# Performance work log

Hardware: AMD Instinct MI355X
Metric: run time of the kernel (lower is better)

Reference implementation:

```python
import jax, jax.numpy as jnp
import numpy as np

N_NODES = 100000
N_EDGES = 500000
HIDDEN = 32
HEADS = 4
PROJ = HIDDEN * HEADS  # 128
LN_EPS = 1e-5


def setup_inputs() -> dict:
    key = jax.random.key(0)
    ks = jax.random.split(key, 12)
    # Xavier-uniform bound for Linear(3, PROJ): sqrt(6/(3+PROJ))
    b_qkv = float(np.sqrt(6.0 / (3 + PROJ)))
    b_out = float(np.sqrt(6.0 / (PROJ + HIDDEN)))
    return {
        "positions": jax.random.normal(ks[0], (N_NODES, 3), dtype=jnp.float32),
        "edge_index": jax.random.randint(ks[1], (2, N_EDGES), 0, N_NODES, dtype=jnp.int64),
        "Wq": jax.random.uniform(ks[2], (3, PROJ), jnp.float32, -b_qkv, b_qkv),
        "bq": jnp.zeros((PROJ,), jnp.float32),
        "Wk": jax.random.uniform(ks[3], (3, PROJ), jnp.float32, -b_qkv, b_qkv),
        "bk": jnp.zeros((PROJ,), jnp.float32),
        "Wv": jax.random.uniform(ks[4], (3, PROJ), jnp.float32, -b_qkv, b_qkv),
        "bv": jnp.zeros((PROJ,), jnp.float32),
        "Wout": jax.random.uniform(ks[5], (PROJ, HIDDEN), jnp.float32, -b_out, b_out),
        "bout": jnp.zeros((HIDDEN,), jnp.float32),
        "gamma": jnp.ones((HIDDEN,), jnp.float32),
        "beta": jnp.zeros((HIDDEN,), jnp.float32),
    }


def reference(positions, edge_index, Wq, bq, Wk, bk, Wv, bv, Wout, bout, gamma, beta):
    row, col = edge_index[0], edge_index[1]
    rel = positions[row] - positions[col]                      # [E, 3]
    E = rel.shape[0]
    q = (rel @ Wq + bq).reshape(E, HEADS, HIDDEN)              # [E, H, D]
    k = (rel @ Wk + bk).reshape(E, HEADS, HIDDEN)
    v = (rel @ Wv + bv).reshape(E, HEADS, HIDDEN)
    # attention score per (edge, head), softmax over heads
    scores = jnp.sum(q * k, axis=-1) / jnp.sqrt(jnp.float32(HIDDEN))  # [E, H]
    attn = jax.nn.softmax(scores, axis=-1)                     # dropout is identity in eval
    wv = (attn[..., None] * v).reshape(E, PROJ)                # [E, H*D]
    # scatter-mean over destination nodes (col), dim_size = N
    seg_sum = jax.ops.segment_sum(wv, col, num_segments=N_NODES)
    counts = jax.ops.segment_sum(jnp.ones((E,), wv.dtype), col, num_segments=N_NODES)
    mean = seg_sum / jnp.maximum(counts, 1.0)[:, None]         # [N, H*D]
    out = mean @ Wout + bout                                   # [N, D]
    mu = jnp.mean(out, axis=-1, keepdims=True)
    var = jnp.var(out, axis=-1, keepdims=True)
    out = (out - mu) / jnp.sqrt(var + LN_EPS) * gamma + beta
    return jax.nn.silu(out)
```

## Files before the change

kernel.cpp:

```cpp
#include <hip/hip_runtime.h>
#include <hip/hip_fp16.h>

#define LN_EPS 1e-5f

typedef _Float16 f16x2 __attribute__((ext_vector_type(2)));
typedef _Float16 f16x8 __attribute__((ext_vector_type(8)));

__device__ __forceinline__ void pk_atomic_add_u32(_Float16* p, unsigned bits) {
  f16x2 v = __builtin_bit_cast(f16x2, bits);
#if __has_builtin(__builtin_amdgcn_flat_atomic_fadd_v2f16)
  __builtin_amdgcn_flat_atomic_fadd_v2f16((f16x2*)p, v);
#else
  unsafeAtomicAdd((__half2*)p, *(__half2*)&v);
#endif
}

__device__ __forceinline__ unsigned pack2(float a, float b) {
  f16x2 v;
  v.x = (_Float16)a;
  v.y = (_Float16)b;
  return __builtin_bit_cast(unsigned, v);
}


__global__ __launch_bounds__(128) void precompute_kernel(
    const float* __restrict__ Wq, const float* __restrict__ bq,
    const float* __restrict__ Wk, const float* __restrict__ bk,
    const float* __restrict__ Wv, const float* __restrict__ bv,
    const float* __restrict__ Wout, float* __restrict__ coef,
    float* __restrict__ T) {
  __shared__ float sW[1024];
  __shared__ float sM[4][3][32];
  __shared__ float sCv[4][32];
  const int t = threadIdx.x;
  const float scale = 0.17677669529663687f;

  if (blockIdx.x == 0) {
    for (int i = t; i < 384; i += 128) {
      sW[i] = Wq[i];
      sW[384 + i] = Wk[i];
    }
    sW[768 + t] = bq[t];
    sW[896 + t] = bk[t];
    __syncthreads();

    if (t < 40) {
      const int h = t / 10, j = t % 10;
      float acc = 0.f;
#pragma unroll 4
      for (int d = 0; d < 32; ++d) {
        const int idx = h * 32 + d;
        float q0 = sW[idx], q1 = sW[128 + idx], q2 = sW[256 + idx];
        float k0 = sW[384 + idx], k1 = sW[512 + idx], k2 = sW[640 + idx];
        float bqv = sW[768 + idx], bkv = sW[896 + idx];
        float v;
        switch (j) {
          case 0: v = q0 * k0; break;
          case 1: v = q1 * k1; break;
          case 2: v = q2 * k2; break;
          case 3: v = q0 * k1 + q1 * k0; break;
          case 4: v = q0 * k2 + q2 * k0; break;
          case 5: v = q1 * k2 + q2 * k1; break;
          case 6: v = q0 * bkv + k0 * bqv; break;
          case 7: v = q1 * bkv + k1 * bqv; break;
          case 8: v = q2 * bkv + k2 * bqv; break;
          default: v = bqv * bkv; break;
        }
        acc += v;
      }
      coef[t] = acc * scale;
    }
  } else {
    const int h = t >> 5, o = t & 31;
    float m0 = 0, m1 = 0, m2 = 0, cv = 0;
    for (int d = 0; d < 32; ++d) {
      const int j = h * 32 + d;
      const float w = Wout[j * 32 + o];
      m0 += Wv[j] * w;
      m1 += Wv[128 + j] * w;
      m2 += Wv[256 + j] * w;
      cv += bv[j] * w;
    }
    sM[h][0][o] = m0;
    sM[h][1][o] = m1;
    sM[h][2][o] = m2;
    sCv[h][o] = cv;
    __syncthreads();

    for (int idx = t; idx < 512; idx += 128) {
      const int j = idx >> 5, col = idx & 31;
      float v;
      if (j < 3)        v = sCv[j][col] - sCv[3][col];
      else if (j < 6)   v = sM[3][j - 3][col];
      else if (j < 15)  { const int h2 = (j - 6) / 3, i = (j - 6) % 3; v = sM[h2][i][col] - sM[3][i][col]; }
      else              v = sCv[3][col];
      T[idx] = v;
    }
  }
}

__global__ __launch_bounds__(256) void edge_kernel(
    const float* __restrict__ pos, const int* __restrict__ ei, int E,
    const float* __restrict__ coef, _Float16* __restrict__ fsums) {
  __shared__ unsigned sF[8][264];
  __shared__ int sC[256];

  const int t = threadIdx.x;
  const int lane64 = t & 63;

  bool pz = true;
  if (lane64 < 8) pz = (ei[2 * lane64 + 1] == 0);
  const unsigned long long bz = __ballot(pz);
  const int i64 = (int)__builtin_amdgcn_readfirstlane(bz == ~0ull ? 1 : 0);

  const int base = blockIdx.x * 256;
  const int vb = min(256, E - base);
  const int e = base + t;

  int c = 0;
  float px0 = 0, px1 = 0, px2 = 0, pc0 = 0, pc1 = 0, pc2 = 0;
  if (t < vb) {
    int r;
    if (i64) {
      r = ((const int2*)ei)[(size_t)e].x;
      c = ((const int2*)ei)[(size_t)E + (size_t)e].x;
    } else {
      r = ei[e];
      c = ei[(size_t)E + e];
    }
    px0 = pos[r * 3 + 0]; px1 = pos[r * 3 + 1]; px2 = pos[r * 3 + 2];
    pc0 = pos[c * 3 + 0]; pc1 = pos[c * 3 + 1]; pc2 = pos[c * 3 + 2];
  }

  if (t < vb) {
    const float rx = px0 - pc0;
    const float ry = px1 - pc1;
    const float rz = px2 - pc2;
    float s[4];
#pragma unroll
    for (int h = 0; h < 4; ++h) {
      const float* cf = coef + h * 10;
      s[h] = cf[9] + rx * cf[6] + ry * cf[7] + rz * cf[8] + rx * rx * cf[0] +
             ry * ry * cf[1] + rz * rz * cf[2] + rx * ry * cf[3] +
             rx * rz * cf[4] + ry * rz * cf[5];
    }
    const float mx = fmaxf(fmaxf(s[0], s[1]), fmaxf(s[2], s[3]));
    const float e0 = __expf(s[0] - mx), e1 = __expf(s[1] - mx);
    const float e2 = __expf(s[2] - mx), e3 = __expf(s[3] - mx);
    const float inv = 1.0f / (e0 + e1 + e2 + e3);
    const float a0 = e0 * inv, a1 = e1 * inv, a2 = e2 * inv;

    sC[t] = c;
    sF[0][t] = pack2(a0, a1);
    sF[1][t] = pack2(a2, rx);
    sF[2][t] = pack2(ry, rz);
    sF[3][t] = pack2(a0 * rx, a0 * ry);
    sF[4][t] = pack2(a0 * rz, a1 * rx);
    sF[5][t] = pack2(a1 * ry, a1 * rz);
    sF[6][t] = pack2(a2 * rx, a2 * ry);
    sF[7][t] = pack2(a2 * rz, 1.0f);
  }
  __syncthreads();

  const int w = t >> 6;
  const int slot = lane64 & 7;
  const int esub = lane64 >> 3;
#pragma unroll
  for (int i = 0; i < 8; ++i) {
    const int g = w * 64 + i * 8 + esub;
    if (g < vb) {
      const int ct = sC[g];
      const unsigned val = sF[slot][g];
      pk_atomic_add_u32(fsums + (size_t)ct * 16 + 2 * slot, val);
    }
  }
}

__global__ __launch_bounds__(256) void node_kernel(
    const _Float16* __restrict__ fsums, const float* __restrict__ T,
    const float* __restrict__ bout, const float* __restrict__ gamma,
    const float* __restrict__ beta, float* __restrict__ out, int N) {
  const int tid = blockIdx.x * blockDim.x + threadIdx.x;
  const int node = tid >> 5;
  const int col = tid & 31;
  if (node >= N) return;

  const f16x8* fp = (const f16x8*)(fsums + (size_t)node * 16);
  const f16x8 va = fp[0];
  const f16x8 vb = fp[1];
  float f[16];
#pragma unroll
  for (int j = 0; j < 8; ++j) {
    f[j] = (float)va[j];
    f[8 + j] = (float)vb[j];
  }
  const float invc = 1.0f / fmaxf(f[15], 1.0f);

  float acc = 0.f;
#pragma unroll
  for (int j = 0; j < 16; ++j) acc = fmaf(f[j], T[j * 32 + col], acc);
  acc = fmaf(acc, invc, bout[col]);

  float sx = acc, sx2 = acc * acc;
#pragma unroll
  for (int off = 16; off >= 1; off >>= 1) {
    sx += __shfl_xor(sx, off);
    sx2 += __shfl_xor(sx2, off);
  }
  const float mu = sx * (1.0f / 32.0f);
  const float var = sx2 * (1.0f / 32.0f) - mu * mu;
  const float inv = rsqrtf(var + LN_EPS);
  const float y = (acc - mu) * inv * gamma[col] + beta[col];
  const float o = y * (1.0f / (1.0f + __expf(-y)));
  out[(size_t)node * 32 + col] = o;
}

extern "C" void kernel_launch(void* const* d_in, const int* in_sizes, int n_in,
                              void* d_out, int out_size, void* d_ws, size_t ws_size,
                              hipStream_t stream) {
  const float* pos  = (const float*)d_in[0];
  const int*   ei   = (const int*)d_in[1];
  const float* Wq   = (const float*)d_in[2];
  const float* bq   = (const float*)d_in[3];
  const float* Wk   = (const float*)d_in[4];
  const float* bk   = (const float*)d_in[5];
  const float* Wv   = (const float*)d_in[6];
  const float* bv   = (const float*)d_in[7];
  const float* Wout = (const float*)d_in[8];
  const float* bout = (const float*)d_in[9];
  const float* gam  = (const float*)d_in[10];
  const float* bet  = (const float*)d_in[11];

  const int N = in_sizes[0] / 3;
  const int E = in_sizes[1] / 2;

  _Float16* fsums = (_Float16*)d_ws;
  float* coef = (float*)((char*)d_ws + (size_t)N * 32);
  float* T = coef + 48;

  hipMemsetAsync(fsums, 0, (size_t)N * 32, stream);

  precompute_kernel<<<2, 128, 0, stream>>>(Wq, bq, Wk, bk, Wv, bv, Wout, coef, T);

  const int edge_blocks = (E + 255) / 256;
  edge_kernel<<<edge_blocks, 256, 0, stream>>>(pos, ei, E, coef, fsums);

  const int node_blocks = (int)(((size_t)N * 32 + 255) / 256);
  node_kernel<<<node_blocks, 256, 0, stream>>>(fsums, T, bout, gam, bet,
                                               (float*)d_out, N);

  (void)n_in; (void)out_size; (void)ws_size;
}
```

Before: 136.7 us.

## Replicate fp16 accumulators across edge blocks and fuse zeroing into precompute kernel

Edge blocks now scatter their atomic adds into one of four replicated fp16 accumulator buffers, chosen by block index, which is meant to reduce atomic contention on the same node addresses. The node kernel sums the four replicas before the projection. The separate memset is replaced by zeroing done inside the precompute kernel, which now launches extra blocks for it. The cost is four times the accumulator memory to zero and read, with more memory traffic and a larger working set.

```diff
diff --git a/kernel.cpp b/kernel.cpp
--- a/kernel.cpp
+++ b/kernel.cpp
@@ -2,6 +2,7 @@
 #include <hip/hip_fp16.h>
 
 #define LN_EPS 1e-5f
+#define NREP 4
 
 typedef _Float16 f16x2 __attribute__((ext_vector_type(2)));
 typedef _Float16 f16x8 __attribute__((ext_vector_type(8)));
@@ -23,12 +24,12 @@
 }
 
 
-__global__ __launch_bounds__(128) void precompute_kernel(
+__global__ __launch_bounds__(256) void precompute_kernel(
     const float* __restrict__ Wq, const float* __restrict__ bq,
     const float* __restrict__ Wk, const float* __restrict__ bk,
     const float* __restrict__ Wv, const float* __restrict__ bv,
     const float* __restrict__ Wout, float* __restrict__ coef,
-    float* __restrict__ T) {
+    float* __restrict__ T, uint4* __restrict__ zbase, int zcount) {
   __shared__ float sW[1024];
   __shared__ float sM[4][3][32];
   __shared__ float sCv[4][32];
@@ -36,12 +37,14 @@
   const float scale = 0.17677669529663687f;
 
   if (blockIdx.x == 0) {
-    for (int i = t; i < 384; i += 128) {
+    for (int i = t; i < 384; i += 256) {
       sW[i] = Wq[i];
       sW[384 + i] = Wk[i];
     }
-    sW[768 + t] = bq[t];
-    sW[896 + t] = bk[t];
+    if (t < 128) {
+      sW[768 + t] = bq[t];
+      sW[896 + t] = bk[t];
+    }
     __syncthreads();
 
     if (t < 40) {
@@ -70,38 +73,47 @@
       }
       coef[t] = acc * scale;
     }
+  } else if (blockIdx.x == 1) {
+    if (t < 128) {
+      const int h = t >> 5, o = t & 31;
+      float m0 = 0, m1 = 0, m2 = 0, cv = 0;
+      for (int d = 0; d < 32; ++d) {
+        const int j = h * 32 + d;
+        const float w = Wout[j * 32 + o];
+        m0 += Wv[j] * w;
+        m1 += Wv[128 + j] * w;
+        m2 += Wv[256 + j] * w;
+        cv += bv[j] * w;
+      }
+      sM[h][0][o] = m0;
+      sM[h][1][o] = m1;
+      sM[h][2][o] = m2;
+      sCv[h][o] = cv;
+    }
+    __syncthreads();
+
+    if (t < 128) {
+      for (int idx = t; idx < 512; idx += 128) {
+        const int j = idx >> 5, col = idx & 31;
+        float v;
+        if (j < 3)        v = sCv[j][col] - sCv[3][col];
+        else if (j < 6)   v = sM[3][j - 3][col];
+        else if (j < 15)  { const int h2 = (j - 6) / 3, i = (j - 6) % 3; v = sM[h2][i][col] - sM[3][i][col]; }
+        else              v = sCv[3][col];
+        T[idx] = v;
+      }
+    }
   } else {
-    const int h = t >> 5, o = t & 31;
-    float m0 = 0, m1 = 0, m2 = 0, cv = 0;
-    for (int d = 0; d < 32; ++d) {
-      const int j = h * 32 + d;
-      const float w = Wout[j * 32 + o];
-      m0 += Wv[j] * w;
-      m1 += Wv[128 + j] * w;
-      m2 += Wv[256 + j] * w;
-      cv += bv[j] * w;
-    }
-    sM[h][0][o] = m0;
-    sM[h][1][o] = m1;
-    sM[h][2][o] = m2;
-    sCv[h][o] = cv;
-    __syncthreads();
-
-    for (int idx = t; idx < 512; idx += 128) {
-      const int j = idx >> 5, col = idx & 31;
-      float v;
-      if (j < 3)        v = sCv[j][col] - sCv[3][col];
-      else if (j < 6)   v = sM[3][j - 3][col];
-      else if (j < 15)  { const int h2 = (j - 6) / 3, i = (j - 6) % 3; v = sM[h2][i][col] - sM[3][i][col]; }
-      else              v = sCv[3][col];
-      T[idx] = v;
-    }
+    const uint4 z = {0u, 0u, 0u, 0u};
+    const int stride = (gridDim.x - 2) * 256;
+    for (int i = (blockIdx.x - 2) * 256 + t; i < zcount; i += stride)
+      zbase[i] = z;
   }
 }
 
 __global__ __launch_bounds__(256) void edge_kernel(
     const float* __restrict__ pos, const int* __restrict__ ei, int E,
-    const float* __restrict__ coef, _Float16* __restrict__ fsums) {
+    const float* __restrict__ coef, _Float16* __restrict__ fsums, int N) {
   __shared__ unsigned sF[8][264];
   __shared__ int sC[256];
 
@@ -162,6 +174,7 @@
   }
   __syncthreads();
 
+  _Float16* fr = fsums + (size_t)(blockIdx.x & (NREP - 1)) * ((size_t)N * 16);
   const int w = t >> 6;
   const int slot = lane64 & 7;
   const int esub = lane64 >> 3;
@@ -171,7 +184,7 @@
     if (g < vb) {
       const int ct = sC[g];
       const unsigned val = sF[slot][g];
-      pk_atomic_add_u32(fsums + (size_t)ct * 16 + 2 * slot, val);
+      pk_atomic_add_u32(fr + (size_t)ct * 16 + 2 * slot, val);
     }
   }
 }
@@ -185,14 +198,20 @@
   const int col = tid & 31;
   if (node >= N) return;
 
-  const f16x8* fp = (const f16x8*)(fsums + (size_t)node * 16);
-  const f16x8 va = fp[0];
-  const f16x8 vb = fp[1];
   float f[16];
 #pragma unroll
-  for (int j = 0; j < 8; ++j) {
-    f[j] = (float)va[j];
-    f[8 + j] = (float)vb[j];
+  for (int j = 0; j < 16; ++j) f[j] = 0.f;
+  const size_t rstride = (size_t)N * 16;
+#pragma unroll
+  for (int r = 0; r < NREP; ++r) {
+    const f16x8* fp = (const f16x8*)(fsums + r * rstride + (size_t)node * 16);
+    const f16x8 va = fp[0];
+    const f16x8 vb = fp[1];
+#pragma unroll
+    for (int j = 0; j < 8; ++j) {
+      f[j] += (float)va[j];
+      f[8 + j] += (float)vb[j];
+    }
   }
   const float invc = 1.0f / fmaxf(f[15], 1.0f);
 
@@ -235,15 +254,15 @@
   const int E = in_sizes[1] / 2;
 
   _Float16* fsums = (_Float16*)d_ws;
-  float* coef = (float*)((char*)d_ws + (size_t)N * 32);
+  float* coef = (float*)((char*)d_ws + (size_t)NREP * N * 32);
   float* T = coef + 48;
 
-  hipMemsetAsync(fsums, 0, (size_t)N * 32, stream);
-
-  precompute_kernel<<<2, 128, 0, stream>>>(Wq, bq, Wk, bk, Wv, bv, Wout, coef, T);
+  const int zcount = (int)(((size_t)NREP * N * 32) / 16);
+  precompute_kernel<<<256, 256, 0, stream>>>(Wq, bq, Wk, bk, Wv, bv, Wout,
+                                             coef, T, (uint4*)d_ws, zcount);
 
   const int edge_blocks = (E + 255) / 256;
-  edge_kernel<<<edge_blocks, 256, 0, stream>>>(pos, ei, E, coef, fsums);
+  edge_kernel<<<edge_blocks, 256, 0, stream>>>(pos, ei, E, coef, fsums, N);
 
   const int node_blocks = (int)(((size_t)N * 32 + 255) / 256);
   node_kernel<<<node_blocks, 256, 0, stream>>>(fsums, T, bout, gam, bet,
```

Result: slower. 145.8 us (+6.7%).
